# Performance work log

Measured on AMD Instinct MI355X. Metric: run time of the kernel, lower is better.

Reference implementation:

```python
import jax, jax.numpy as jnp
import numpy as np
from jax.ops import segment_sum, segment_max

N = 100000          # nodes
E = 1600000         # edges
F_NODE = 128
F_EDGE = 32
HID = 64
ACT = 32
NG = 1000           # graph rows in y (repeat_factor = N // NG = 100)
NEG_SLOPE = 0.2


def _add_self_loops(src, dst, ea, n):
    # PyG add_self_loops with fill_value='mean': self-loop attr = mean of
    # incoming edge_attr per target node (0 for isolated nodes).
    cnt = segment_sum(jnp.ones((ea.shape[0],), ea.dtype), dst, num_segments=n)
    loop_attr = segment_sum(ea, dst, num_segments=n) / jnp.clip(cnt, 1.0)[:, None]
    ar = jnp.arange(n, dtype=src.dtype)
    return (jnp.concatenate([src, ar]),
            jnp.concatenate([dst, ar]),
            jnp.concatenate([ea, loop_attr], axis=0))


def _gatv2(xx, src, dst, ea, Wl, bl, Wr, br, We, att, bias, n):
    xl = xx @ Wl + bl                      # source transform  [n, HID]
    xr = xx @ Wr + br                      # target transform  [n, HID]
    e = ea @ We                            # edge embedding    [E', HID]
    m = jax.nn.leaky_relu(xl[src] + xr[dst] + e, NEG_SLOPE)
    logits = m @ att                       # [E']
    mx = segment_max(logits, dst, num_segments=n)
    ex = jnp.exp(logits - mx[dst])
    den = segment_sum(ex, dst, num_segments=n)
    alpha = ex / den[dst]                  # segment softmax over incoming edges
    return segment_sum(xl[src] * alpha[:, None], dst, num_segments=n) + bias


def setup_inputs() -> dict:
    key = jax.random.key(0)
    ks = jax.random.split(key, 32)
    g = lambda k, s: jax.random.normal(k, s, jnp.float32)
    p = lambda k, s: jax.random.normal(k, s, jnp.float32) * 0.05
    return {
        "x": g(ks[0], (N, F_NODE)),
        "edge_attr": g(ks[1], (E, F_EDGE)),
        "y": g(ks[2], (2 * NG,)),
        "Wl1": p(ks[3], (F_NODE, HID)), "bl1": p(ks[4], (HID,)),
        "Wr1": p(ks[5], (F_NODE, HID)), "br1": p(ks[6], (HID,)),
        "We1": p(ks[7], (F_EDGE, HID)), "att1": p(ks[8], (HID,)),
        "bias1": p(ks[9], (HID,)),
        "Wl2": p(ks[10], (HID, HID)), "bl2": p(ks[11], (HID,)),
        "Wr2": p(ks[12], (HID, HID)), "br2": p(ks[13], (HID,)),
        "We2": p(ks[14], (F_EDGE, HID)), "att2": p(ks[15], (HID,)),
        "bias2": p(ks[16], (HID,)),
        "W0": p(ks[17], (2, 2)), "b0": p(ks[18], (2,)),
        "W1": p(ks[19], (HID + 2, 32)), "b1": p(ks[20], (32,)),
        "W2": p(ks[21], (32, ACT)), "b2": p(ks[22], (ACT,)),
        "edge_index": jax.random.randint(ks[23], (2, E), 0, N),
        "node_idx": jax.random.randint(ks[24], (1000,), 0, N),
    }


def reference(x, edge_attr, y, Wl1, bl1, Wr1, br1, We1, att1, bias1,
              Wl2, bl2, Wr2, br2, We2, att2, bias2,
              W0, b0, W1, b1, W2, b2, edge_index, node_idx):
    n = x.shape[0]
    src, dst, ea = _add_self_loops(edge_index[0], edge_index[1], edge_attr, n)
    h = jax.nn.relu(_gatv2(x, src, dst, ea, Wl1, bl1, Wr1, br1, We1, att1, bias1, n))
    h = jax.nn.relu(_gatv2(h, src, dst, ea, Wl2, bl2, Wr2, br2, We2, att2, bias2, n))
    yr = y.reshape(-1, 2)
    repeat_factor = n // yr.shape[0]
    yr = jnp.repeat(yr, repeat_factor, axis=0)          # [n, 2]
    yr = jax.nn.relu(yr @ W0 + b0)
    z = jnp.concatenate([h, yr], axis=1)                # [n, HID+2]
    z = jax.nn.relu(z @ W1 + b1)
    z = z @ W2 + b2                                     # [n, ACT]
    return z[node_idx]
```

## Files before the change

kernel.cpp:

```cpp
#include <hip/hip_runtime.h>


#define NF1CAP 24576

__device__ __forceinline__ int getbit(const unsigned* b, int i) {
    return (b[i >> 5] >> (i & 31)) & 1;
}

__global__ __launch_bounds__(256)
void mark_sel_kernel(const int* __restrict__ nidx, unsigned* __restrict__ selbits,
                     unsigned* __restrict__ f1bits, int n)
{
    int t = blockIdx.x * blockDim.x + threadIdx.x;
    if (t < n) {
        int i = nidx[t];
        atomicOr(&selbits[i >> 5], 1u << (i & 31));
        atomicOr(&f1bits[i >> 5], 1u << (i & 31));
    }
}

__global__ __launch_bounds__(256)
void pass_a_kernel(const int* __restrict__ src, const int* __restrict__ dst,
                   const unsigned* __restrict__ selbits,
                   unsigned* __restrict__ f1bits, int* __restrict__ indeg, int E)
{
    int E4 = E >> 2;
    for (int i = blockIdx.x * blockDim.x + threadIdx.x; i < E4;
         i += gridDim.x * blockDim.x) {
        int4 d4 = ((const int4*)dst)[i];
        int dd[4] = {d4.x, d4.y, d4.z, d4.w};
#pragma unroll
        for (int j = 0; j < 4; ++j) {
            int d = dd[j];
            atomicAdd(&indeg[d], 1);
            if (getbit(selbits, d)) {
                int s = src[i * 4 + j];
                atomicOr(&f1bits[s >> 5], 1u << (s & 31));
            }
        }
    }
    int t = blockIdx.x * blockDim.x + threadIdx.x;
    if (t < (E & 3)) {
        int e = (E4 << 2) + t;
        int d = dst[e];
        atomicAdd(&indeg[d], 1);
        if (getbit(selbits, d)) {
            int s = src[e];
            atomicOr(&f1bits[s >> 5], 1u << (s & 31));
        }
    }
}

__global__ __launch_bounds__(256)
void compact_f1_kernel(const unsigned* __restrict__ f1bits, int* __restrict__ nf1,
                       int* __restrict__ f1node, int* __restrict__ slot_of, int n)
{
    int i = blockIdx.x * blockDim.x + threadIdx.x;
    if (i >= n) return;
    if (getbit(f1bits, i)) {
        int s = atomicAdd(nf1, 1);
        if (s < NF1CAP) { f1node[s] = i; slot_of[i] = s; }
        else slot_of[i] = 0;
    }
}

__global__ __launch_bounds__(1024)
void scan_kernel(const int* __restrict__ indeg, const int* __restrict__ f1node,
                 const int* __restrict__ n_ptr, int cap,
                 int* __restrict__ offs, int* __restrict__ ne_out)
{
    __shared__ int buf[1024];
    int n = *n_ptr; if (n > cap) n = cap;
    int tid = threadIdx.x;
    int chunk = (n + 1023) / 1024;
    int base = tid * chunk;
    int s = 0;
    for (int j = 0; j < chunk; ++j) {
        int idx = base + j;
        if (idx < n) s += indeg[f1node[idx]];
    }
    buf[tid] = s;
    __syncthreads();
    for (int off = 1; off < 1024; off <<= 1) {
        int v = (tid >= off) ? buf[tid - off] : 0;
        __syncthreads();
        buf[tid] += v;
        __syncthreads();
    }
    int run = (tid > 0) ? buf[tid - 1] : 0;
    for (int j = 0; j < chunk; ++j) {
        int idx = base + j;
        if (idx < n) { offs[idx] = run; run += indeg[f1node[idx]]; }
    }
    if (tid == 1023) { offs[n] = buf[1023]; *ne_out = buf[1023]; }
}

__global__ __launch_bounds__(256)
void scatter_kernel(const int* __restrict__ src, const int* __restrict__ dst,
                    const unsigned* __restrict__ f1bits,
                    const int* __restrict__ slot_of, const int* __restrict__ aoffs,
                    int* __restrict__ cursor,
                    unsigned long long* __restrict__ apack, int E)
{
    int E4 = E >> 2;
    for (int i = blockIdx.x * blockDim.x + threadIdx.x; i < E4;
         i += gridDim.x * blockDim.x) {
        int4 d4 = ((const int4*)dst)[i];
        int dd[4] = {d4.x, d4.y, d4.z, d4.w};
#pragma unroll
        for (int j = 0; j < 4; ++j) {
            int d = dd[j];
            if (!getbit(f1bits, d)) continue;
            int a = slot_of[d];
            int pos = aoffs[a] + atomicAdd(&cursor[a], 1);
            int e = i * 4 + j;
            apack[pos] = (unsigned long long)(unsigned)e
                       | ((unsigned long long)(unsigned)src[e] << 21)
                       | ((unsigned long long)(unsigned)a << 38);
        }
    }
    int t = blockIdx.x * blockDim.x + threadIdx.x;
    if (t < (E & 3)) {
        int e = (E4 << 2) + t;
        int d = dst[e];
        if (getbit(f1bits, d)) {
            int a = slot_of[d];
            int pos = aoffs[a] + atomicAdd(&cursor[a], 1);
            apack[pos] = (unsigned long long)(unsigned)e
                       | ((unsigned long long)(unsigned)src[e] << 21)
                       | ((unsigned long long)(unsigned)a << 38);
        }
    }
}

template <int K>
__global__ __launch_bounds__(256)
void gemm_tiled_kernel(const float* __restrict__ X,
                       const float* __restrict__ W, const float* __restrict__ bias,
                       const int* __restrict__ rowlist,
                       const int* __restrict__ nrows_p, int nrows_fixed, int cap,
                       float* __restrict__ out)
{
    constexpr int BM = 128, BK = 32, LDA = BM + 4;
    __shared__ float sW[K * 64];
    __shared__ float sA[BK * LDA];
    int rows = nrows_p ? *nrows_p : nrows_fixed;
    if (rows > cap) rows = cap;
    int base = (int)blockIdx.x * BM;
    if (base >= rows) return;
    int tid = threadIdx.x;
    for (int t = tid; t < K * 16; t += 256)
        ((float4*)sW)[t] = ((const float4*)W)[t];
    int tx = tid & 7, ty = tid >> 3;
    int c0 = tx * 8;
    float acc[4][8];
#pragma unroll
    for (int i = 0; i < 4; ++i)
#pragma unroll
        for (int j = 0; j < 8; ++j) acc[i][j] = 0.f;

    for (int kb = 0; kb < K; kb += BK) {
        __syncthreads();
#pragma unroll
        for (int q = 0; q < 4; ++q) {
            int lin = q * 256 + tid;
            int m = lin >> 3;
            int kk = (lin & 7) * 4;
            int rr = base + m;
            if (rr >= rows) rr = rows - 1;
            int grow = rowlist ? rowlist[rr] : rr;
            float4 v = *(const float4*)&X[(size_t)grow * K + kb + kk];
            sA[(kk + 0) * LDA + m] = v.x;
            sA[(kk + 1) * LDA + m] = v.y;
            sA[(kk + 2) * LDA + m] = v.z;
            sA[(kk + 3) * LDA + m] = v.w;
        }
        __syncthreads();
#pragma unroll
        for (int k = 0; k < BK; ++k) {
            float4 a4 = *(const float4*)&sA[k * LDA + ty * 4];
            float4 w0 = *(const float4*)&sW[(kb + k) * 64 + c0];
            float4 w1 = *(const float4*)&sW[(kb + k) * 64 + c0 + 4];
            float av[4] = {a4.x, a4.y, a4.z, a4.w};
            float wv[8] = {w0.x, w0.y, w0.z, w0.w, w1.x, w1.y, w1.z, w1.w};
#pragma unroll
            for (int i = 0; i < 4; ++i)
#pragma unroll
                for (int j = 0; j < 8; ++j)
                    acc[i][j] += av[i] * wv[j];
        }
    }
    float bv[8];
#pragma unroll
    for (int j = 0; j < 8; ++j) bv[j] = bias[c0 + j];
#pragma unroll
    for (int i = 0; i < 4; ++i) {
        int r = base + ty * 4 + i;
        if (r < rows) {
            float o[8];
#pragma unroll
            for (int j = 0; j < 8; ++j) o[j] = acc[i][j] + bv[j];
            *(float4*)&out[(size_t)r * 64 + c0] = *(float4*)&o[0];
            *(float4*)&out[(size_t)r * 64 + c0 + 4] = *(float4*)&o[4];
        }
    }
}

__global__ __launch_bounds__(256)
void logits1_kernel(const int* __restrict__ ne_ptr,
                    const unsigned long long* __restrict__ apack,
                    const float* __restrict__ eattr, const float* __restrict__ xl,
                    const float* __restrict__ xrc, const float* __restrict__ We,
                    const float* __restrict__ att, float* __restrict__ alogit)
{
    constexpr int LDE = 36;
    __shared__ float sAttr[64 * LDE];
    int tid = threadIdx.x;
    int lane = tid & 63, w = tid >> 6;
    float wec[32];
#pragma unroll
    for (int k = 0; k < 32; ++k) wec[k] = We[k * 64 + lane];
    float att_l = att[lane];
    int n = *ne_ptr;
    int ntiles = (n + 63) >> 6;
    for (int tile = blockIdx.x; tile < ntiles; tile += gridDim.x) {
        int base = tile << 6;
        __syncthreads();
#pragma unroll
        for (int q = 0; q < 2; ++q) {
            int lin = q * 256 + tid;
            int el = lin >> 3, quad = lin & 7;
            int p = base + el; if (p >= n) p = n - 1;
            int e = (int)(apack[p] & 0x1FFFFF);
            float4 v = ((const float4*)(eattr + (size_t)e * 32))[quad];
            *(float4*)&sAttr[el * LDE + quad * 4] = v;
        }
        __syncthreads();
        float res = 0.f;
#pragma unroll
        for (int j0 = 0; j0 < 16; j0 += 4) {
            float xlv[4], xrv[4];
#pragma unroll
            for (int u = 0; u < 4; ++u) {
                int p = base + w * 16 + j0 + u; if (p >= n) p = n - 1;
                unsigned long long rec = apack[p];
                int s = (int)((rec >> 21) & 0x1FFFF);
                int a = (int)((rec >> 38) & 0x7FFF);
                xlv[u] = xl[(size_t)s * 64 + lane];
                xrv[u] = xrc[(size_t)a * 64 + lane];
            }
#pragma unroll
            for (int u = 0; u < 4; ++u) {
                int el = w * 16 + j0 + u;
                const float* ar = &sAttr[el * LDE];
                float emb = 0.f;
#pragma unroll
                for (int k = 0; k < 32; ++k) emb += ar[k] * wec[k];
                float m = xlv[u] + xrv[u] + emb;
                m = (m >= 0.f) ? m : 0.2f * m;
                float pf = m * att_l;
#pragma unroll
                for (int d = 32; d; d >>= 1) pf += __shfl_xor(pf, d, 64);
                res = (lane == j0 + u) ? pf : res;
            }
        }
        int li = base + w * 16 + lane;
        if (lane < 16 && li < n) alogit[li] = res;
    }
}

__global__ __launch_bounds__(256)
void logits2_kernel(const int* __restrict__ nidx, const int* __restrict__ slot_of,
                    const int* __restrict__ aoffs,
                    const unsigned long long* __restrict__ apack,
                    const float* __restrict__ eattr, const float* __restrict__ xl2c,
                    const float* __restrict__ xr2c, const float* __restrict__ We,
                    const float* __restrict__ att, float* __restrict__ alogit,
                    int nsel)
{
    int lane = threadIdx.x & 63;
    int w = (blockIdx.x * blockDim.x + threadIdx.x) >> 6;
    int item = w >> 4, sub = w & 15;
    if (item >= nsel) return;
    float wec[32];
#pragma unroll
    for (int k = 0; k < 32; ++k) wec[k] = We[k * 64 + lane];
    float att_l = att[lane];
    int i = nidx[item];
    int a = slot_of[i];
    int beg = aoffs[a], end = aoffs[a + 1];
    float xr_l = xr2c[(size_t)a * 64 + lane];
    for (int p = beg + sub; p < end; p += 16) {
        unsigned long long rec = apack[p];
        int e = (int)(rec & 0x1FFFFF);
        int s = (int)((rec >> 21) & 0x1FFFF);
        const float4* a4 = (const float4*)(eattr + (size_t)e * 32);
        float emb = 0.f;
#pragma unroll
        for (int q = 0; q < 8; ++q) {
            float4 v = a4[q];
            emb += v.x * wec[4 * q] + v.y * wec[4 * q + 1]
                 + v.z * wec[4 * q + 2] + v.w * wec[4 * q + 3];
        }
        float m = xl2c[(size_t)slot_of[s] * 64 + lane] + xr_l + emb;
        m = (m >= 0.f) ? m : 0.2f * m;
        float pf = m * att_l;
#pragma unroll
        for (int d = 32; d; d >>= 1) pf += __shfl_xor(pf, d, 64);
        if (lane == 0) alogit[p] = pf;
    }
}

__global__ __launch_bounds__(256)
void sc1_kernel(const int* __restrict__ nf1_p, const int* __restrict__ f1node,
                const int* __restrict__ aoffs,
                const unsigned long long* __restrict__ apack,
                const float* __restrict__ eattr, float* __restrict__ mattr,
                const float* __restrict__ xl1, const float* __restrict__ xr1c,
                const float* __restrict__ We, const float* __restrict__ att,
                const float* __restrict__ alogit, const float* __restrict__ bias,
                float* __restrict__ h1c)
{
    int lane = threadIdx.x & 63, l32 = lane & 31, half = lane >> 5;
    int gw = (blockIdx.x * blockDim.x + threadIdx.x) >> 6;
    int nw = (gridDim.x * blockDim.x) >> 6;
    float wec[32];
#pragma unroll
    for (int k = 0; k < 32; ++k) wec[k] = We[k * 64 + lane];
    float att_l = att[lane];
    float bias_l = bias[lane];
    int n = *nf1_p; if (n > NF1CAP) n = NF1CAP;
    for (int a = gw; a < n; a += nw) {
        int i = f1node[a];
        int beg = aoffs[a], end = aoffs[a + 1], deg = end - beg;
        float ls = 0.f;
        for (int p = beg + half; p < end; p += 2) {
            int e = (int)(apack[p] & 0x1FFFFF);
            ls += eattr[(size_t)e * 32 + l32];
        }
        ls += __shfl_xor(ls, 32, 64);
        float mean = ls * (1.0f / (float)(deg > 0 ? deg : 1));
        if (lane < 32) mattr[(size_t)a * 32 + lane] = mean;
        float emb = 0.f;
#pragma unroll
        for (int k = 0; k < 32; ++k) emb += __shfl(mean, k, 64) * wec[k];
        float xls = xl1[(size_t)i * 64 + lane];
        float m = xls + xr1c[(size_t)a * 64 + lane] + emb;
        m = (m >= 0.f) ? m : 0.2f * m;
        float pf = m * att_l;
#pragma unroll
        for (int d = 32; d; d >>= 1) pf += __shfl_xor(pf, d, 64);
        float slog = pf;
        float mx = slog;
        for (int p = beg + lane; p < end; p += 64) mx = fmaxf(mx, alogit[p]);
#pragma unroll
        for (int d = 32; d; d >>= 1) mx = fmaxf(mx, __shfl_xor(mx, d, 64));
        float ps = 0.f;
        for (int p = beg + lane; p < end; p += 64) ps += __expf(alogit[p] - mx);
#pragma unroll
        for (int d = 32; d; d >>= 1) ps += __shfl_xor(ps, d, 64);
        float wself = __expf(slog - mx);
        float den = ps + wself;
        float o0 = wself * xls, o1 = 0.f;
        int p = beg;
        for (; p + 2 <= end; p += 2) {
            unsigned long long r0 = apack[p], r1 = apack[p + 1];
            float w0 = __expf(alogit[p] - mx);
            float w1 = __expf(alogit[p + 1] - mx);
            int s0 = (int)((r0 >> 21) & 0x1FFFF);
            int s1 = (int)((r1 >> 21) & 0x1FFFF);
            o0 += w0 * xl1[(size_t)s0 * 64 + lane];
            o1 += w1 * xl1[(size_t)s1 * 64 + lane];
        }
        if (p < end) {
            float wgt = __expf(alogit[p] - mx);
            int s = (int)((apack[p] >> 21) & 0x1FFFF);
            o0 += wgt * xl1[(size_t)s * 64 + lane];
        }
        h1c[(size_t)a * 64 + lane] = fmaxf((o0 + o1) / den + bias_l, 0.f);
    }
}

__global__ __launch_bounds__(256)
void tail2_kernel(const int* __restrict__ nidx, const int* __restrict__ slot_of,
                  const int* __restrict__ aoffs,
                  const unsigned long long* __restrict__ apack,
                  const float* __restrict__ mattr, const float* __restrict__ xl2c,
                  const float* __restrict__ xr2c, const float* __restrict__ We,
                  const float* __restrict__ att, const float* __restrict__ alogit,
                  const float* __restrict__ bias, const float* __restrict__ y,
                  const float* __restrict__ W0, const float* __restrict__ b0,
                  const float* __restrict__ W1, const float* __restrict__ b1,
                  const float* __restrict__ W2, const float* __restrict__ b2,
                  float* __restrict__ out, int nsel, int rf)
{
    int lane = threadIdx.x & 63;
    int r = (blockIdx.x * blockDim.x + threadIdx.x) >> 6;
    if (r >= nsel) return;
    float wec[32];
#pragma unroll
    for (int k = 0; k < 32; ++k) wec[k] = We[k * 64 + lane];
    float att_l = att[lane];
    float bias_l = bias[lane];
    int i = nidx[r];
    int a = slot_of[i];
    int beg = aoffs[a], end = aoffs[a + 1];
    float mean = mattr[(size_t)a * 32 + (lane & 31)];
    float emb = 0.f;
#pragma unroll
    for (int k = 0; k < 32; ++k) emb += __shfl(mean, k, 64) * wec[k];
    float xls = xl2c[(size_t)a * 64 + lane];
    float m = xls + xr2c[(size_t)a * 64 + lane] + emb;
    m = (m >= 0.f) ? m : 0.2f * m;
    float pf = m * att_l;
#pragma unroll
    for (int d = 32; d; d >>= 1) pf += __shfl_xor(pf, d, 64);
    float slog = pf;
    float mx = slog;
    for (int p = beg + lane; p < end; p += 64) mx = fmaxf(mx, alogit[p]);
#pragma unroll
    for (int d = 32; d; d >>= 1) mx = fmaxf(mx, __shfl_xor(mx, d, 64));
    float ps = 0.f;
    for (int p = beg + lane; p < end; p += 64) ps += __expf(alogit[p] - mx);
#pragma unroll
    for (int d = 32; d; d >>= 1) ps += __shfl_xor(ps, d, 64);
    float wself = __expf(slog - mx);
    float den = ps + wself;
    float o = wself * xls;
    for (int p = beg; p < end; ++p) {
        float wgt = __expf(alogit[p] - mx);
        int s = (int)((apack[p] >> 21) & 0x1FFFF);
        o += wgt * xl2c[(size_t)slot_of[s] * 64 + lane];
    }
    float h = fmaxf(o / den + bias_l, 0.f);
    int yi = i / rf;
    float y0 = y[2 * yi], y1 = y[2 * yi + 1];
    float t0 = fmaxf(y0 * W0[0] + y1 * W0[2] + b0[0], 0.f);
    float t1 = fmaxf(y0 * W0[1] + y1 * W0[3] + b0[1], 0.f);
    int j = lane & 31;
    float acc = b1[j];
#pragma unroll
    for (int k = 0; k < 64; ++k) acc += __shfl(h, k, 64) * W1[k * 32 + j];
    acc += t0 * W1[64 * 32 + j] + t1 * W1[65 * 32 + j];
    acc = fmaxf(acc, 0.f);
    float res = b2[j];
#pragma unroll
    for (int k = 0; k < 32; ++k) res += __shfl(acc, k, 64) * W2[k * 32 + j];
    if (lane < 32) out[(size_t)r * 32 + j] = res;
}

extern "C" void kernel_launch(void* const* d_in, const int* in_sizes, int n_in,
                              void* d_out, int out_size, void* d_ws,
                              size_t ws_size, hipStream_t stream)
{
    const float* x     = (const float*)d_in[0];
    const float* eattr = (const float*)d_in[1];
    const float* y     = (const float*)d_in[2];
    const float* Wl1 = (const float*)d_in[3],  *bl1 = (const float*)d_in[4];
    const float* Wr1 = (const float*)d_in[5],  *br1 = (const float*)d_in[6];
    const float* We1 = (const float*)d_in[7],  *att1 = (const float*)d_in[8];
    const float* bias1 = (const float*)d_in[9];
    const float* Wl2 = (const float*)d_in[10], *bl2 = (const float*)d_in[11];
    const float* Wr2 = (const float*)d_in[12], *br2 = (const float*)d_in[13];
    const float* We2 = (const float*)d_in[14], *att2 = (const float*)d_in[15];
    const float* bias2 = (const float*)d_in[16];
    const float* W0 = (const float*)d_in[17], *b0 = (const float*)d_in[18];
    const float* W1 = (const float*)d_in[19], *b1 = (const float*)d_in[20];
    const float* W2 = (const float*)d_in[21], *b2 = (const float*)d_in[22];
    const int* eidx = (const int*)d_in[23];
    const int* nidx = (const int*)d_in[24];

    const int N = in_sizes[0] / 128;
    const int E = in_sizes[1] / 32;
    const int NSEL = in_sizes[24];
    const int NGr = in_sizes[2] / 2;
    const int rf = N / NGr;

    const int* src = eidx;
    const int* dst = eidx + E;

    size_t off = 0;
    auto alloc = [&](size_t nb) {
        size_t r = off;
        off += (nb + 255) & ~(size_t)255;
        return r;
    };
    char* ws = (char*)d_ws;
    const int NBW = (N + 31) / 32;

    unsigned* selbits = (unsigned*)(ws + alloc((size_t)NBW * 4));
    unsigned* f1bits  = (unsigned*)(ws + alloc((size_t)NBW * 4));
    int* indeg  = (int*)(ws + alloc((size_t)N * 4));
    int* cursor = (int*)(ws + alloc((size_t)NF1CAP * 4));
    int* ctrs   = (int*)(ws + alloc(256));
    size_t zero_bytes = off;
    int* slot_of = (int*)(ws + alloc((size_t)N * 4));
    int* f1node  = (int*)(ws + alloc((size_t)NF1CAP * 4));
    int* aoffs   = (int*)(ws + alloc((size_t)(NF1CAP + 1) * 4));
    unsigned long long* apack =
        (unsigned long long*)(ws + alloc((size_t)E * 8));
    float* alogit = (float*)(ws + alloc((size_t)E * 4));
    float* mattr  = (float*)(ws + alloc((size_t)NF1CAP * 32 * 4));
    float* xl1  = (float*)(ws + alloc((size_t)N * 64 * 4));
    float* xr1c = (float*)(ws + alloc((size_t)NF1CAP * 64 * 4));
    float* h1c  = (float*)(ws + alloc((size_t)NF1CAP * 64 * 4));
    float* xl2c = (float*)(ws + alloc((size_t)NF1CAP * 64 * 4));
    float* xr2c = (float*)(ws + alloc((size_t)NF1CAP * 64 * 4));
    (void)ws_size;

    int* nf1_p = ctrs + 0;
    int* ne1_p = ctrs + 1;

    hipMemsetAsync(ws, 0, zero_bytes, stream);

    mark_sel_kernel<<<(NSEL + 255) / 256, 256, 0, stream>>>(nidx, selbits,
                                                            f1bits, NSEL);
    pass_a_kernel<<<2048, 256, 0, stream>>>(src, dst, selbits, f1bits, indeg, E);
    compact_f1_kernel<<<(N + 255) / 256, 256, 0, stream>>>(f1bits, nf1_p,
                                                           f1node, slot_of, N);
    scan_kernel<<<1, 1024, 0, stream>>>(indeg, f1node, nf1_p, NF1CAP, aoffs,
                                        ne1_p);
    scatter_kernel<<<2048, 256, 0, stream>>>(src, dst, f1bits, slot_of, aoffs,
                                             cursor, apack, E);
    gemm_tiled_kernel<128><<<(N + 127) / 128, 256, 0, stream>>>(
        x, Wl1, bl1, nullptr, nullptr, N, N, xl1);
    gemm_tiled_kernel<128><<<NF1CAP / 128, 256, 0, stream>>>(
        x, Wr1, br1, f1node, nf1_p, 0, NF1CAP, xr1c);
    logits1_kernel<<<2048, 256, 0, stream>>>(ne1_p, apack, eattr, xl1, xr1c,
                                             We1, att1, alogit);
    sc1_kernel<<<4096, 256, 0, stream>>>(nf1_p, f1node, aoffs, apack, eattr,
                                         mattr, xl1, xr1c, We1, att1, alogit,
                                         bias1, h1c);
    gemm_tiled_kernel<64><<<NF1CAP / 128, 256, 0, stream>>>(
        h1c, Wl2, bl2, nullptr, nf1_p, 0, NF1CAP, xl2c);
    gemm_tiled_kernel<64><<<NF1CAP / 128, 256, 0, stream>>>(
        h1c, Wr2, br2, nullptr, nf1_p, 0, NF1CAP, xr2c);
    logits2_kernel<<<NSEL * 4, 256, 0, stream>>>(nidx, slot_of, aoffs, apack,
                                                 eattr, xl2c, xr2c, We2, att2,
                                                 alogit, NSEL);
    tail2_kernel<<<(NSEL + 3) / 4, 256, 0, stream>>>(
        nidx, slot_of, aoffs, apack, mattr, xl2c, xr2c, We2, att2, alogit,
        bias2, y, W0, b0, W1, b1, W2, b2, (float*)d_out, NSEL, rf);
}
```

Measured before the change: 689.0 us.

## Fuse edge logits into online-softmax aggregation kernels and merge GEMM launches

Removes the separate per-edge logits kernels and the alogit/mattr buffers: each block now handles one target node, computes edge logits, the self-loop mean attribute, and an online (streaming) softmax-weighted aggregation in a single pass. The two layer-1 GEMMs are merged into one launch, and the layer-2 Wl/Wr GEMMs share one A-tile load. This cuts kernel launches and global round trips of logits, but assigns a whole 256-thread block per node, which is idle for low-degree nodes and adds many barriers.

After: 670.5 us. 1.03x faster.

```diff
diff --git a/kernel.cpp b/kernel.cpp
--- a/kernel.cpp
+++ b/kernel.cpp
@@ -133,20 +133,28 @@
     }
 }
 
-template <int K>
-__global__ __launch_bounds__(256)
-void gemm_tiled_kernel(const float* __restrict__ X,
-                       const float* __restrict__ W, const float* __restrict__ bias,
-                       const int* __restrict__ rowlist,
-                       const int* __restrict__ nrows_p, int nrows_fixed, int cap,
-                       float* __restrict__ out)
-{
-    constexpr int BM = 128, BK = 32, LDA = BM + 4;
+__global__ __launch_bounds__(256)
+void gemm1_fused_kernel(const float* __restrict__ X,
+                        const float* __restrict__ Wl, const float* __restrict__ bl,
+                        const float* __restrict__ Wr, const float* __restrict__ br,
+                        const int* __restrict__ f1node,
+                        const int* __restrict__ nf1_p,
+                        int ndense, int gb_dense,
+                        float* __restrict__ outl, float* __restrict__ outr)
+{
+    constexpr int K = 128, BM = 128, BK = 32, LDA = BM + 4;
     __shared__ float sW[K * 64];
     __shared__ float sA[BK * LDA];
-    int rows = nrows_p ? *nrows_p : nrows_fixed;
-    if (rows > cap) rows = cap;
-    int base = (int)blockIdx.x * BM;
+    bool dense = (int)blockIdx.x < gb_dense;
+    const float* W = dense ? Wl : Wr;
+    const float* bias = dense ? bl : br;
+    const int* rowlist = dense ? nullptr : f1node;
+    float* out = dense ? outl : outr;
+    int rows;
+    if (dense) rows = ndense;
+    else { rows = *nf1_p; if (rows > NF1CAP) rows = NF1CAP; }
+    int bid = dense ? (int)blockIdx.x : (int)blockIdx.x - gb_dense;
+    int base = bid * BM;
     if (base >= rows) return;
     int tid = threadIdx.x;
     for (int t = tid; t < K * 16; t += 256)
@@ -207,177 +215,216 @@
 }
 
 __global__ __launch_bounds__(256)
-void logits1_kernel(const int* __restrict__ ne_ptr,
-                    const unsigned long long* __restrict__ apack,
-                    const float* __restrict__ eattr, const float* __restrict__ xl,
-                    const float* __restrict__ xrc, const float* __restrict__ We,
-                    const float* __restrict__ att, float* __restrict__ alogit)
+void gemm2_both_kernel(const float* __restrict__ X,
+                       const float* __restrict__ Wl, const float* __restrict__ bl,
+                       const float* __restrict__ Wr, const float* __restrict__ br,
+                       const int* __restrict__ nf1_p,
+                       float* __restrict__ outl, float* __restrict__ outr)
+{
+    constexpr int K = 64, BM = 128, BK = 32, LDA = BM + 4;
+    __shared__ float sW[2 * K * 64];
+    __shared__ float sA[BK * LDA];
+    int rows = *nf1_p; if (rows > NF1CAP) rows = NF1CAP;
+    int base = (int)blockIdx.x * BM;
+    if (base >= rows) return;
+    int tid = threadIdx.x;
+    for (int t = tid; t < K * 16; t += 256) {
+        ((float4*)sW)[t] = ((const float4*)Wl)[t];
+        ((float4*)sW)[K * 16 + t] = ((const float4*)Wr)[t];
+    }
+    int tx = tid & 7, ty = tid >> 3;
+    int c0 = tx * 8;
+    float accl[4][8], accr[4][8];
+#pragma unroll
+    for (int i = 0; i < 4; ++i)
+#pragma unroll
+        for (int j = 0; j < 8; ++j) { accl[i][j] = 0.f; accr[i][j] = 0.f; }
+
+    for (int kb = 0; kb < K; kb += BK) {
+        __syncthreads();
+#pragma unroll
+        for (int q = 0; q < 4; ++q) {
+            int lin = q * 256 + tid;
+            int m = lin >> 3;
+            int kk = (lin & 7) * 4;
+            int rr = base + m;
+            if (rr >= rows) rr = rows - 1;
+            float4 v = *(const float4*)&X[(size_t)rr * K + kb + kk];
+            sA[(kk + 0) * LDA + m] = v.x;
+            sA[(kk + 1) * LDA + m] = v.y;
+            sA[(kk + 2) * LDA + m] = v.z;
+            sA[(kk + 3) * LDA + m] = v.w;
+        }
+        __syncthreads();
+#pragma unroll
+        for (int k = 0; k < BK; ++k) {
+            float4 a4 = *(const float4*)&sA[k * LDA + ty * 4];
+            float4 l0 = *(const float4*)&sW[(kb + k) * 64 + c0];
+            float4 l1 = *(const float4*)&sW[(kb + k) * 64 + c0 + 4];
+            float4 r0 = *(const float4*)&sW[K * 64 + (kb + k) * 64 + c0];
+            float4 r1 = *(const float4*)&sW[K * 64 + (kb + k) * 64 + c0 + 4];
+            float av[4] = {a4.x, a4.y, a4.z, a4.w};
+            float lv[8] = {l0.x, l0.y, l0.z, l0.w, l1.x, l1.y, l1.z, l1.w};
+            float rv[8] = {r0.x, r0.y, r0.z, r0.w, r1.x, r1.y, r1.z, r1.w};
+#pragma unroll
+            for (int i = 0; i < 4; ++i)
+#pragma unroll
+                for (int j = 0; j < 8; ++j) {
+                    accl[i][j] += av[i] * lv[j];
+                    accr[i][j] += av[i] * rv[j];
+                }
+        }
+    }
+    float blv[8], brv[8];
+#pragma unroll
+    for (int j = 0; j < 8; ++j) { blv[j] = bl[c0 + j]; brv[j] = br[c0 + j]; }
+#pragma unroll
+    for (int i = 0; i < 4; ++i) {
+        int r = base + ty * 4 + i;
+        if (r < rows) {
+            float ol[8], orr[8];
+#pragma unroll
+            for (int j = 0; j < 8; ++j) {
+                ol[j] = accl[i][j] + blv[j];
+                orr[j] = accr[i][j] + brv[j];
+            }
+            *(float4*)&outl[(size_t)r * 64 + c0] = *(float4*)&ol[0];
+            *(float4*)&outl[(size_t)r * 64 + c0 + 4] = *(float4*)&ol[4];
+            *(float4*)&outr[(size_t)r * 64 + c0] = *(float4*)&orr[0];
+            *(float4*)&outr[(size_t)r * 64 + c0 + 4] = *(float4*)&orr[4];
+        }
+    }
+}
+
+__global__ __launch_bounds__(256)
+void agg1_kernel(const int* __restrict__ nf1_p, const int* __restrict__ f1node,
+                 const int* __restrict__ aoffs,
+                 const unsigned long long* __restrict__ apack,
+                 const float* __restrict__ eattr,
+                 const float* __restrict__ xl, const float* __restrict__ xrc,
+                 const float* __restrict__ We, const float* __restrict__ att,
+                 const float* __restrict__ bias, float* __restrict__ h1c)
 {
     constexpr int LDE = 36;
     __shared__ float sAttr[64 * LDE];
-    int tid = threadIdx.x;
-    int lane = tid & 63, w = tid >> 6;
+    __shared__ int   sSrc[64];
+    __shared__ int   sEid[64];
+    __shared__ float sLog[64];
+    __shared__ float sRedM[4], sRedD[4];
+    __shared__ float sCol[8][32];
+    __shared__ float sMean[32];
+    __shared__ float sAcc[4][64];
+
+    int tid = threadIdx.x, lane = tid & 63, w = tid >> 6;
     float wec[32];
 #pragma unroll
     for (int k = 0; k < 32; ++k) wec[k] = We[k * 64 + lane];
-    float att_l = att[lane];
-    int n = *ne_ptr;
-    int ntiles = (n + 63) >> 6;
-    for (int tile = blockIdx.x; tile < ntiles; tile += gridDim.x) {
-        int base = tile << 6;
-        __syncthreads();
-#pragma unroll
-        for (int q = 0; q < 2; ++q) {
-            int lin = q * 256 + tid;
-            int el = lin >> 3, quad = lin & 7;
-            int p = base + el; if (p >= n) p = n - 1;
-            int e = (int)(apack[p] & 0x1FFFFF);
-            float4 v = ((const float4*)(eattr + (size_t)e * 32))[quad];
-            *(float4*)&sAttr[el * LDE + quad * 4] = v;
-        }
-        __syncthreads();
-        float res = 0.f;
-#pragma unroll
-        for (int j0 = 0; j0 < 16; j0 += 4) {
-            float xlv[4], xrv[4];
-#pragma unroll
-            for (int u = 0; u < 4; ++u) {
-                int p = base + w * 16 + j0 + u; if (p >= n) p = n - 1;
-                unsigned long long rec = apack[p];
-                int s = (int)((rec >> 21) & 0x1FFFF);
-                int a = (int)((rec >> 38) & 0x7FFF);
-                xlv[u] = xl[(size_t)s * 64 + lane];
-                xrv[u] = xrc[(size_t)a * 64 + lane];
-            }
-#pragma unroll
-            for (int u = 0; u < 4; ++u) {
-                int el = w * 16 + j0 + u;
-                const float* ar = &sAttr[el * LDE];
+    float att_l = att[lane], bias_l = bias[lane];
+    int n = *nf1_p; if (n > NF1CAP) n = NF1CAP;
+
+    for (int a = blockIdx.x; a < n; a += gridDim.x) {
+        int i = f1node[a];
+        int beg = aoffs[a], deg = aoffs[a + 1] - beg;
+        float xl_i = xl[(size_t)i * 64 + lane];
+        float xr_i = xrc[(size_t)a * 64 + lane];
+        float run_m = -3.0e38f, run_den = 0.f, accw = 0.f, colsum = 0.f;
+
+        for (int t0 = 0; t0 < deg; t0 += 64) {
+            int tn = deg - t0; if (tn > 64) tn = 64;
+            __syncthreads();
+            if (tid < tn) {
+                unsigned long long rec = apack[beg + t0 + tid];
+                sEid[tid] = (int)(rec & 0x1FFFFF);
+                sSrc[tid] = (int)((rec >> 21) & 0x1FFFF);
+            }
+            __syncthreads();
+#pragma unroll
+            for (int q = 0; q < 2; ++q) {
+                int lin = q * 256 + tid;
+                int el = lin >> 3, quad = lin & 7;
+                if (el < tn) {
+                    float4 v = ((const float4*)(eattr
+                                 + (size_t)sEid[el] * 32))[quad];
+                    *(float4*)&sAttr[el * LDE + quad * 4] = v;
+                }
+            }
+            __syncthreads();
+            for (int r = tid >> 5; r < tn; r += 8)
+                colsum += sAttr[r * LDE + (tid & 31)];
+            for (int j = w; j < tn; j += 4) {
+                const float* ar = &sAttr[j * LDE];
                 float emb = 0.f;
 #pragma unroll
                 for (int k = 0; k < 32; ++k) emb += ar[k] * wec[k];
-                float m = xlv[u] + xrv[u] + emb;
+                float m = xl[(size_t)sSrc[j] * 64 + lane] + xr_i + emb;
                 m = (m >= 0.f) ? m : 0.2f * m;
                 float pf = m * att_l;
 #pragma unroll
                 for (int d = 32; d; d >>= 1) pf += __shfl_xor(pf, d, 64);
-                res = (lane == j0 + u) ? pf : res;
-            }
-        }
-        int li = base + w * 16 + lane;
-        if (lane < 16 && li < n) alogit[li] = res;
-    }
-}
-
-__global__ __launch_bounds__(256)
-void logits2_kernel(const int* __restrict__ nidx, const int* __restrict__ slot_of,
-                    const int* __restrict__ aoffs,
-                    const unsigned long long* __restrict__ apack,
-                    const float* __restrict__ eattr, const float* __restrict__ xl2c,
-                    const float* __restrict__ xr2c, const float* __restrict__ We,
-                    const float* __restrict__ att, float* __restrict__ alogit,
-                    int nsel)
-{
-    int lane = threadIdx.x & 63;
-    int w = (blockIdx.x * blockDim.x + threadIdx.x) >> 6;
-    int item = w >> 4, sub = w & 15;
-    if (item >= nsel) return;
-    float wec[32];
-#pragma unroll
-    for (int k = 0; k < 32; ++k) wec[k] = We[k * 64 + lane];
-    float att_l = att[lane];
-    int i = nidx[item];
-    int a = slot_of[i];
-    int beg = aoffs[a], end = aoffs[a + 1];
-    float xr_l = xr2c[(size_t)a * 64 + lane];
-    for (int p = beg + sub; p < end; p += 16) {
-        unsigned long long rec = apack[p];
-        int e = (int)(rec & 0x1FFFFF);
-        int s = (int)((rec >> 21) & 0x1FFFF);
-        const float4* a4 = (const float4*)(eattr + (size_t)e * 32);
-        float emb = 0.f;
-#pragma unroll
-        for (int q = 0; q < 8; ++q) {
-            float4 v = a4[q];
-            emb += v.x * wec[4 * q] + v.y * wec[4 * q + 1]
-                 + v.z * wec[4 * q + 2] + v.w * wec[4 * q + 3];
-        }
-        float m = xl2c[(size_t)slot_of[s] * 64 + lane] + xr_l + emb;
-        m = (m >= 0.f) ? m : 0.2f * m;
-        float pf = m * att_l;
-#pragma unroll
-        for (int d = 32; d; d >>= 1) pf += __shfl_xor(pf, d, 64);
-        if (lane == 0) alogit[p] = pf;
-    }
-}
-
-__global__ __launch_bounds__(256)
-void sc1_kernel(const int* __restrict__ nf1_p, const int* __restrict__ f1node,
-                const int* __restrict__ aoffs,
-                const unsigned long long* __restrict__ apack,
-                const float* __restrict__ eattr, float* __restrict__ mattr,
-                const float* __restrict__ xl1, const float* __restrict__ xr1c,
-                const float* __restrict__ We, const float* __restrict__ att,
-                const float* __restrict__ alogit, const float* __restrict__ bias,
-                float* __restrict__ h1c)
-{
-    int lane = threadIdx.x & 63, l32 = lane & 31, half = lane >> 5;
-    int gw = (blockIdx.x * blockDim.x + threadIdx.x) >> 6;
-    int nw = (gridDim.x * blockDim.x) >> 6;
-    float wec[32];
-#pragma unroll
-    for (int k = 0; k < 32; ++k) wec[k] = We[k * 64 + lane];
-    float att_l = att[lane];
-    float bias_l = bias[lane];
-    int n = *nf1_p; if (n > NF1CAP) n = NF1CAP;
-    for (int a = gw; a < n; a += nw) {
-        int i = f1node[a];
-        int beg = aoffs[a], end = aoffs[a + 1], deg = end - beg;
-        float ls = 0.f;
-        for (int p = beg + half; p < end; p += 2) {
-            int e = (int)(apack[p] & 0x1FFFFF);
-            ls += eattr[(size_t)e * 32 + l32];
-        }
-        ls += __shfl_xor(ls, 32, 64);
-        float mean = ls * (1.0f / (float)(deg > 0 ? deg : 1));
-        if (lane < 32) mattr[(size_t)a * 32 + lane] = mean;
-        float emb = 0.f;
-#pragma unroll
-        for (int k = 0; k < 32; ++k) emb += __shfl(mean, k, 64) * wec[k];
-        float xls = xl1[(size_t)i * 64 + lane];
-        float m = xls + xr1c[(size_t)a * 64 + lane] + emb;
-        m = (m >= 0.f) ? m : 0.2f * m;
-        float pf = m * att_l;
+                if (lane == 0) sLog[j] = pf;
+            }
+            __syncthreads();
+            float wm = (tid < tn) ? sLog[tid] : -3.0e38f;
+#pragma unroll
+            for (int d = 32; d; d >>= 1) wm = fmaxf(wm, __shfl_xor(wm, d, 64));
+            if (lane == 0) sRedM[w] = wm;
+            __syncthreads();
+            float bm = fmaxf(fmaxf(sRedM[0], sRedM[1]),
+                             fmaxf(sRedM[2], sRedM[3]));
+            float newm = fmaxf(run_m, bm);
+            float dp = (tid < tn) ? __expf(sLog[tid] - newm) : 0.f;
+#pragma unroll
+            for (int d = 32; d; d >>= 1) dp += __shfl_xor(dp, d, 64);
+            if (lane == 0) sRedD[w] = dp;
+            __syncthreads();
+            float bden = sRedD[0] + sRedD[1] + sRedD[2] + sRedD[3];
+            float sc = __expf(run_m - newm);
+            accw *= sc;
+            run_den = run_den * sc + bden;
+            int j = w;
+            for (; j + 8 <= tn + w; j += 8) {
+                int j1 = j + 4;
+                float w0 = __expf(sLog[j] - newm);
+                float v0 = xl[(size_t)sSrc[j] * 64 + lane];
+                float w1 = (j1 < tn) ? __expf(sLog[j1] - newm) : 0.f;
+                float v1 = (j1 < tn) ? xl[(size_t)sSrc[j1] * 64 + lane] : 0.f;
+                accw += w0 * v0;
+                accw += w1 * v1;
+            }
+            for (; j < tn; j += 4) {
+                float wgt = __expf(sLog[j] - newm);
+                accw += wgt * xl[(size_t)sSrc[j] * 64 + lane];
+            }
+            run_m = newm;
+        }
+        sCol[tid >> 5][tid & 31] = colsum;
+        __syncthreads();
+        if (tid < 32) {
+            float s = 0.f;
+#pragma unroll
+            for (int r = 0; r < 8; ++r) s += sCol[r][tid];
+            sMean[tid] = s / (float)(deg > 0 ? deg : 1);
+        }
+        __syncthreads();
+        float embs = 0.f;
+#pragma unroll
+        for (int k = 0; k < 32; ++k) embs += sMean[k] * wec[k];
+        float ms = xl_i + xr_i + embs;
+        ms = (ms >= 0.f) ? ms : 0.2f * ms;
+        float pf = ms * att_l;
 #pragma unroll
         for (int d = 32; d; d >>= 1) pf += __shfl_xor(pf, d, 64);
         float slog = pf;
-        float mx = slog;
-        for (int p = beg + lane; p < end; p += 64) mx = fmaxf(mx, alogit[p]);
-#pragma unroll
-        for (int d = 32; d; d >>= 1) mx = fmaxf(mx, __shfl_xor(mx, d, 64));
-        float ps = 0.f;
-        for (int p = beg + lane; p < end; p += 64) ps += __expf(alogit[p] - mx);
-#pragma unroll
-        for (int d = 32; d; d >>= 1) ps += __shfl_xor(ps, d, 64);
-        float wself = __expf(slog - mx);
-        float den = ps + wself;
-        float o0 = wself * xls, o1 = 0.f;
-        int p = beg;
-        for (; p + 2 <= end; p += 2) {
-            unsigned long long r0 = apack[p], r1 = apack[p + 1];
-            float w0 = __expf(alogit[p] - mx);
-            float w1 = __expf(alogit[p + 1] - mx);
-            int s0 = (int)((r0 >> 21) & 0x1FFFF);
-            int s1 = (int)((r1 >> 21) & 0x1FFFF);
-            o0 += w0 * xl1[(size_t)s0 * 64 + lane];
-            o1 += w1 * xl1[(size_t)s1 * 64 + lane];
-        }
-        if (p < end) {
-            float wgt = __expf(alogit[p] - mx);
-            int s = (int)((apack[p] >> 21) & 0x1FFFF);
-            o0 += wgt * xl1[(size_t)s * 64 + lane];
-        }
-        h1c[(size_t)a * 64 + lane] = fmaxf((o0 + o1) / den + bias_l, 0.f);
+        float newm = fmaxf(run_m, slog);
+        float sc = __expf(run_m - newm);
+        float wself = __expf(slog - newm);
+        float den = run_den * sc + wself;
+        sAcc[w][lane] = accw * sc;
+        __syncthreads();
+        float tot = sAcc[0][lane] + sAcc[1][lane] + sAcc[2][lane]
+                  + sAcc[3][lane] + wself * xl_i;
+        h1c[(size_t)a * 64 + lane] = fmaxf(tot / den + bias_l, 0.f);
+        __syncthreads();
     }
 }
 
@@ -385,68 +432,140 @@
 void tail2_kernel(const int* __restrict__ nidx, const int* __restrict__ slot_of,
                   const int* __restrict__ aoffs,
                   const unsigned long long* __restrict__ apack,
-                  const float* __restrict__ mattr, const float* __restrict__ xl2c,
-                  const float* __restrict__ xr2c, const float* __restrict__ We,
-                  const float* __restrict__ att, const float* __restrict__ alogit,
+                  const float* __restrict__ eattr,
+                  const float* __restrict__ xl2c, const float* __restrict__ xr2c,
+                  const float* __restrict__ We, const float* __restrict__ att,
                   const float* __restrict__ bias, const float* __restrict__ y,
                   const float* __restrict__ W0, const float* __restrict__ b0,
                   const float* __restrict__ W1, const float* __restrict__ b1,
                   const float* __restrict__ W2, const float* __restrict__ b2,
                   float* __restrict__ out, int nsel, int rf)
 {
-    int lane = threadIdx.x & 63;
-    int r = (blockIdx.x * blockDim.x + threadIdx.x) >> 6;
-    if (r >= nsel) return;
+    constexpr int LDE = 36;
+    __shared__ float sAttr[64 * LDE];
+    __shared__ int   sSrc[64];
+    __shared__ int   sEid[64];
+    __shared__ float sLog[64];
+    __shared__ float sRedM[4], sRedD[4];
+    __shared__ float sCol[8][32];
+    __shared__ float sMean[32];
+    __shared__ float sAcc[4][64];
+
+    int tid = threadIdx.x, lane = tid & 63, w = tid >> 6;
     float wec[32];
 #pragma unroll
     for (int k = 0; k < 32; ++k) wec[k] = We[k * 64 + lane];
-    float att_l = att[lane];
-    float bias_l = bias[lane];
-    int i = nidx[r];
-    int a = slot_of[i];
-    int beg = aoffs[a], end = aoffs[a + 1];
-    float mean = mattr[(size_t)a * 32 + (lane & 31)];
-    float emb = 0.f;
-#pragma unroll
-    for (int k = 0; k < 32; ++k) emb += __shfl(mean, k, 64) * wec[k];
-    float xls = xl2c[(size_t)a * 64 + lane];
-    float m = xls + xr2c[(size_t)a * 64 + lane] + emb;
-    m = (m >= 0.f) ? m : 0.2f * m;
-    float pf = m * att_l;
-#pragma unroll
-    for (int d = 32; d; d >>= 1) pf += __shfl_xor(pf, d, 64);
-    float slog = pf;
-    float mx = slog;
-    for (int p = beg + lane; p < end; p += 64) mx = fmaxf(mx, alogit[p]);
-#pragma unroll
-    for (int d = 32; d; d >>= 1) mx = fmaxf(mx, __shfl_xor(mx, d, 64));
-    float ps = 0.f;
-    for (int p = beg + lane; p < end; p += 64) ps += __expf(alogit[p] - mx);
-#pragma unroll
-    for (int d = 32; d; d >>= 1) ps += __shfl_xor(ps, d, 64);
-    float wself = __expf(slog - mx);
-    float den = ps + wself;
-    float o = wself * xls;
-    for (int p = beg; p < end; ++p) {
-        float wgt = __expf(alogit[p] - mx);
-        int s = (int)((apack[p] >> 21) & 0x1FFFF);
-        o += wgt * xl2c[(size_t)slot_of[s] * 64 + lane];
-    }
-    float h = fmaxf(o / den + bias_l, 0.f);
-    int yi = i / rf;
-    float y0 = y[2 * yi], y1 = y[2 * yi + 1];
-    float t0 = fmaxf(y0 * W0[0] + y1 * W0[2] + b0[0], 0.f);
-    float t1 = fmaxf(y0 * W0[1] + y1 * W0[3] + b0[1], 0.f);
-    int j = lane & 31;
-    float acc = b1[j];
-#pragma unroll
-    for (int k = 0; k < 64; ++k) acc += __shfl(h, k, 64) * W1[k * 32 + j];
-    acc += t0 * W1[64 * 32 + j] + t1 * W1[65 * 32 + j];
-    acc = fmaxf(acc, 0.f);
-    float res = b2[j];
-#pragma unroll
-    for (int k = 0; k < 32; ++k) res += __shfl(acc, k, 64) * W2[k * 32 + j];
-    if (lane < 32) out[(size_t)r * 32 + j] = res;
+    float att_l = att[lane], bias_l = bias[lane];
+
+    for (int r = blockIdx.x; r < nsel; r += gridDim.x) {
+        int i = nidx[r];
+        int a = slot_of[i];
+        int beg = aoffs[a], deg = aoffs[a + 1] - beg;
+        float xl_i = xl2c[(size_t)a * 64 + lane];
+        float xr_i = xr2c[(size_t)a * 64 + lane];
+        float run_m = -3.0e38f, run_den = 0.f, accw = 0.f, colsum = 0.f;
+
+        for (int t0 = 0; t0 < deg; t0 += 64) {
+            int tn = deg - t0; if (tn > 64) tn = 64;
+            __syncthreads();
+            if (tid < tn) {
+                unsigned long long rec = apack[beg + t0 + tid];
+                sEid[tid] = (int)(rec & 0x1FFFFF);
+                sSrc[tid] = slot_of[(int)((rec >> 21) & 0x1FFFF)];
+            }
+            __syncthreads();
+#pragma unroll
+            for (int q = 0; q < 2; ++q) {
+                int lin = q * 256 + tid;
+                int el = lin >> 3, quad = lin & 7;
+                if (el < tn) {
+                    float4 v = ((const float4*)(eattr
+                                 + (size_t)sEid[el] * 32))[quad];
+                    *(float4*)&sAttr[el * LDE + quad * 4] = v;
+                }
+            }
+            __syncthreads();
+            for (int rr = tid >> 5; rr < tn; rr += 8)
+                colsum += sAttr[rr * LDE + (tid & 31)];
+            for (int j = w; j < tn; j += 4) {
+                const float* ar = &sAttr[j * LDE];
+                float emb = 0.f;
+#pragma unroll
+                for (int k = 0; k < 32; ++k) emb += ar[k] * wec[k];
+                float m = xl2c[(size_t)sSrc[j] * 64 + lane] + xr_i + emb;
+                m = (m >= 0.f) ? m : 0.2f * m;
+                float pf = m * att_l;
+#pragma unroll
+                for (int d = 32; d; d >>= 1) pf += __shfl_xor(pf, d, 64);
+                if (lane == 0) sLog[j] = pf;
+            }
+            __syncthreads();
+            float wm = (tid < tn) ? sLog[tid] : -3.0e38f;
+#pragma unroll
+            for (int d = 32; d; d >>= 1) wm = fmaxf(wm, __shfl_xor(wm, d, 64));
+            if (lane == 0) sRedM[w] = wm;
+            __syncthreads();
+            float bm = fmaxf(fmaxf(sRedM[0], sRedM[1]),
+                             fmaxf(sRedM[2], sRedM[3]));
+            float newm = fmaxf(run_m, bm);
+            float dp = (tid < tn) ? __expf(sLog[tid] - newm) : 0.f;
+#pragma unroll
+            for (int d = 32; d; d >>= 1) dp += __shfl_xor(dp, d, 64);
+            if (lane == 0) sRedD[w] = dp;
+            __syncthreads();
+            float bden = sRedD[0] + sRedD[1] + sRedD[2] + sRedD[3];
+            float sc = __expf(run_m - newm);
+            accw *= sc;
+            run_den = run_den * sc + bden;
+            for (int j = w; j < tn; j += 4) {
+                float wgt = __expf(sLog[j] - newm);
+                accw += wgt * xl2c[(size_t)sSrc[j] * 64 + lane];
+            }
+            run_m = newm;
+        }
+        sCol[tid >> 5][tid & 31] = colsum;
+        __syncthreads();
+        if (tid < 32) {
+            float s = 0.f;
+#pragma unroll
+            for (int rr = 0; rr < 8; ++rr) s += sCol[rr][tid];
+            sMean[tid] = s / (float)(deg > 0 ? deg : 1);
+        }
+        __syncthreads();
+        float embs = 0.f;
+#pragma unroll
+        for (int k = 0; k < 32; ++k) embs += sMean[k] * wec[k];
+        float ms = xl_i + xr_i + embs;
+        ms = (ms >= 0.f) ? ms : 0.2f * ms;
+        float pf = ms * att_l;
+#pragma unroll
+        for (int d = 32; d; d >>= 1) pf += __shfl_xor(pf, d, 64);
+        float slog = pf;
+        float newm = fmaxf(run_m, slog);
+        float sc = __expf(run_m - newm);
+        float wself = __expf(slog - newm);
+        float den = run_den * sc + wself;
+        sAcc[w][lane] = accw * sc;
+        __syncthreads();
+        float tot = sAcc[0][lane] + sAcc[1][lane] + sAcc[2][lane]
+                  + sAcc[3][lane] + wself * xl_i;
+        float h = fmaxf(tot / den + bias_l, 0.f);
+        int yi = i / rf;
+        float y0 = y[2 * yi], y1 = y[2 * yi + 1];
+        float t0v = fmaxf(y0 * W0[0] + y1 * W0[2] + b0[0], 0.f);
+        float t1v = fmaxf(y0 * W0[1] + y1 * W0[3] + b0[1], 0.f);
+        int j = lane & 31;
+        float acc = b1[j];
+#pragma unroll
+        for (int k = 0; k < 64; ++k) acc += __shfl(h, k, 64) * W1[k * 32 + j];
+        acc += t0v * W1[64 * 32 + j] + t1v * W1[65 * 32 + j];
+        acc = fmaxf(acc, 0.f);
+        float res = b2[j];
+#pragma unroll
+        for (int k = 0; k < 32; ++k) res += __shfl(acc, k, 64) * W2[k * 32 + j];
+        if (w == 0 && lane < 32) out[(size_t)r * 32 + j] = res;
+        __syncthreads();
+    }
 }
 
 extern "C" void kernel_launch(void* const* d_in, const int* in_sizes, int n_in,
@@ -499,8 +618,6 @@
     int* aoffs   = (int*)(ws + alloc((size_t)(NF1CAP + 1) * 4));
     unsigned long long* apack =
         (unsigned long long*)(ws + alloc((size_t)E * 8));
-    float* alogit = (float*)(ws + alloc((size_t)E * 4));
-    float* mattr  = (float*)(ws + alloc((size_t)NF1CAP * 32 * 4));
     float* xl1  = (float*)(ws + alloc((size_t)N * 64 * 4));
     float* xr1c = (float*)(ws + alloc((size_t)NF1CAP * 64 * 4));
     float* h1c  = (float*)(ws + alloc((size_t)NF1CAP * 64 * 4));
@@ -522,23 +639,18 @@
                                         ne1_p);
     scatter_kernel<<<2048, 256, 0, stream>>>(src, dst, f1bits, slot_of, aoffs,
                                              cursor, apack, E);
-    gemm_tiled_kernel<128><<<(N + 127) / 128, 256, 0, stream>>>(
-        x, Wl1, bl1, nullptr, nullptr, N, N, xl1);
-    gemm_tiled_kernel<128><<<NF1CAP / 128, 256, 0, stream>>>(
-        x, Wr1, br1, f1node, nf1_p, 0, NF1CAP, xr1c);
-    logits1_kernel<<<2048, 256, 0, stream>>>(ne1_p, apack, eattr, xl1, xr1c,
-                                             We1, att1, alogit);
-    sc1_kernel<<<4096, 256, 0, stream>>>(nf1_p, f1node, aoffs, apack, eattr,
-                                         mattr, xl1, xr1c, We1, att1, alogit,
-                                         bias1, h1c);
-    gemm_tiled_kernel<64><<<NF1CAP / 128, 256, 0, stream>>>(
-        h1c, Wl2, bl2, nullptr, nf1_p, 0, NF1CAP, xl2c);
-    gemm_tiled_kernel<64><<<NF1CAP / 128, 256, 0, stream>>>(
-        h1c, Wr2, br2, nullptr, nf1_p, 0, NF1CAP, xr2c);
-    logits2_kernel<<<NSEL * 4, 256, 0, stream>>>(nidx, slot_of, aoffs, apack,
-                                                 eattr, xl2c, xr2c, We2, att2,
-                                                 alogit, NSEL);
-    tail2_kernel<<<(NSEL + 3) / 4, 256, 0, stream>>>(
-        nidx, slot_of, aoffs, apack, mattr, xl2c, xr2c, We2, att2, alogit,
-        bias2, y, W0, b0, W1, b1, W2, b2, (float*)d_out, NSEL, rf);
-}
+    {
+        int gb_dense = (N + 127) / 128;
+        int gb_total = gb_dense + NF1CAP / 128;
+        gemm1_fused_kernel<<<gb_total, 256, 0, stream>>>(
+            x, Wl1, bl1, Wr1, br1, f1node, nf1_p, N, gb_dense, xl1, xr1c);
+    }
+    agg1_kernel<<<4096, 256, 0, stream>>>(nf1_p, f1node, aoffs, apack, eattr,
+                                          xl1, xr1c, We1, att1, bias1, h1c);
+    gemm2_both_kernel<<<NF1CAP / 128, 256, 0, stream>>>(h1c, Wl2, bl2, Wr2,
+                                                        br2, nf1_p, xl2c, xr2c);
+    tail2_kernel<<<NSEL, 256, 0, stream>>>(nidx, slot_of, aoffs, apack, eattr,
+                                           xl2c, xr2c, We2, att2, bias2, y,
+                                           W0, b0, W1, b1, W2, b2,
+                                           (float*)d_out, NSEL, rf);
+}
```
